# Kernel optimization log

Measured on AMD Instinct MI355X. Metric: run time of the kernel, lower is better.

Reference implementation:

```python
import jax, jax.numpy as jnp
import numpy as np

NUM_NODES = 50000
NUM_EDGES = 800000
NUM_LABEL_EDGES = 100000
F_IN, F_HID, F_OUT = 128, 128, 64


def gcn_conv(x, src, dst, W, b, n):
    # PyG GCNConv: h = x @ W; add self-loops; symmetric normalization
    # deg counted on destination (col), including self-loop (+1).
    h = x @ W
    deg = jax.ops.segment_sum(jnp.ones(src.shape, h.dtype), dst, num_segments=n) + 1.0
    dinv = jax.lax.rsqrt(deg)  # deg >= 1 always (self-loop)
    norm = dinv[src] * dinv[dst]                       # [E]
    agg = jax.ops.segment_sum(h[src] * norm[:, None], dst, num_segments=n)
    agg = agg + h * (dinv * dinv)[:, None]             # self-loop term dinv[i]^2 * h[i]
    return agg + b


def setup_inputs() -> dict:
    key = jax.random.key(0)
    ks = jax.random.split(key, 9)
    x = jax.random.normal(ks[0], (NUM_NODES, F_IN), dtype=jnp.float32)
    edge_index = jax.random.randint(ks[1], (2, NUM_EDGES), 0, NUM_NODES, dtype=jnp.int64)
    edge_label_index = jax.random.randint(ks[2], (2, NUM_LABEL_EDGES), 0, NUM_NODES, dtype=jnp.int64)
    def glorot(k, fi, fo):
        s = (6.0 / (fi + fo)) ** 0.5
        return jax.random.uniform(k, (fi, fo), jnp.float32, -s, s)
    return {
        "x": x,
        "edge_index": edge_index,
        "edge_label_index": edge_label_index,
        "W1": glorot(ks[3], F_IN, F_HID),  "b1": jnp.zeros((F_HID,), jnp.float32),
        "W2": glorot(ks[4], F_HID, F_HID), "b2": jnp.zeros((F_HID,), jnp.float32),
        "W3": glorot(ks[5], F_HID, F_OUT), "b3": jnp.zeros((F_OUT,), jnp.float32),
    }


def reference(x, edge_index, edge_label_index, W1, b1, W2, b2, W3, b3):
    src, dst = edge_index[0], edge_index[1]
    z = jax.nn.relu(gcn_conv(x, src, dst, W1, b1, NUM_NODES))
    z = jax.nn.relu(gcn_conv(z, src, dst, W2, b2, NUM_NODES))
    z = gcn_conv(z, src, dst, W3, b3, NUM_NODES)
    # decode: dot product of endpoint embeddings per label edge
    return jnp.sum(z[edge_label_index[0]] * z[edge_label_index[1]], axis=-1)
```

## Files before the change

### kernel.cpp

```cpp
#include <hip/hip_runtime.h>
#include <hip/hip_bf16.h>
#include <stdint.h>

#define NN 50000
#define NE 800000
#define NL 100000
#define SLOTS 64

#define NB 196
#define BSH 8
#define BCAP 5376

typedef __attribute__((ext_vector_type(8))) short bf16x8;
typedef __attribute__((ext_vector_type(4))) float f32x4;
typedef __attribute__((ext_vector_type(4))) unsigned int u32x4;

__device__ __forceinline__ float asf(unsigned int u) {
    union { unsigned int i; float f; } c; c.i = u; return c.f;
}
__device__ __forceinline__ float bflo(unsigned int x) { return asf(x << 16); }
__device__ __forceinline__ float bfhi(unsigned int x) { return asf(x & 0xffff0000u); }
__device__ __forceinline__ unsigned short f2bf(float f) {
    union { float f; unsigned int i; } c; c.f = f;
    unsigned int u = c.i + (0x7fffu + ((c.i >> 16) & 1u));
    return (unsigned short)(u >> 16);
}

__global__ void k_wprep(const float* __restrict__ W1, const float* __restrict__ W2,
                        const float* __restrict__ W3, unsigned short* __restrict__ Wt,
                        int* __restrict__ cursor) {
    int idx = blockIdx.x * 256 + threadIdx.x;
    if (idx < NB) cursor[idx] = 0;
    const float* W; unsigned short* O; int base, Mloc;
    if (idx < 16384)      { W = W1; O = Wt;         base = idx;         Mloc = 128; }
    else if (idx < 32768) { W = W2; O = Wt + 16384; base = idx - 16384; Mloc = 128; }
    else                  { W = W3; O = Wt + 32768; base = idx - 32768; Mloc = 64;  }
    int n = base >> 7, k = base & 127;
    O[base] = f2bf(W[k * Mloc + n]);
}

__global__ __launch_bounds__(256) void k_bin(
        const int* __restrict__ src, const int* __restrict__ dst,
        int* __restrict__ cursor, unsigned int* __restrict__ binbuf) {
    __shared__ int hcnt[NB];
    __shared__ int hbase[NB];
    __shared__ unsigned int epk[2048];
    int tid = threadIdx.x;
    if (tid < NB) hcnt[tid] = 0;
    __syncthreads();
    int e0 = blockIdx.x * 2048;
    int e1 = min(e0 + 2048, NE);
    for (int e = e0 + tid; e < e1; e += 256) {
        int d = dst[e], s = src[e];
        atomicAdd(&hcnt[d >> BSH], 1);
        epk[e - e0] = (unsigned int)s | ((unsigned int)d << 16);
    }
    __syncthreads();
    if (tid < NB) { hbase[tid] = atomicAdd(&cursor[tid], hcnt[tid]); hcnt[tid] = 0; }
    __syncthreads();
    for (int e = e0 + tid; e < e1; e += 256) {
        unsigned int pk = epk[e - e0];
        int b = (int)(pk >> 16) >> BSH;
        int p = hbase[b] + atomicAdd(&hcnt[b], 1);
        if (p < BCAP)
            __builtin_nontemporal_store(pk, &binbuf[(size_t)b * BCAP + p]);
    }
}

__global__ __launch_bounds__(256) void k_csr(
        const unsigned int* __restrict__ binbuf, const int* __restrict__ cursor,
        int* __restrict__ deg, unsigned short* __restrict__ colp) {
    __shared__ unsigned short lcol[256 * SLOTS];
    __shared__ int ldeg[256];
    int tid = threadIdx.x;
    int blk = blockIdx.x;
    int base = blk << BSH;
    int nNodes = min(256, NN - base);
    ldeg[tid] = 0;
    __syncthreads();
    int cnt = min(cursor[blk], BCAP);
    for (int e = tid; e < cnt; e += 256) {
        unsigned int pk = __builtin_nontemporal_load(&binbuf[(size_t)blk * BCAP + e]);
        int d = (int)(pk >> 16) - base;
        int p = atomicAdd(&ldeg[d], 1);
        if (p < SLOTS) lcol[d * SLOTS + p] = (unsigned short)(pk & 0xffffu);
    }
    __syncthreads();
    if (tid < nNodes) deg[base + tid] = ldeg[tid];
    u32x4* gout = (u32x4*)(colp + (size_t)base * SLOTS);
    const u32x4* lin = (const u32x4*)lcol;
    for (int i = tid; i < nNodes * 8; i += 256) gout[i] = lin[i];
}

__global__ __launch_bounds__(256) void k_gemm1(
        const float* __restrict__ A, const unsigned short* __restrict__ Wt,
        const int* __restrict__ deg, unsigned short* __restrict__ Outb, int N) {
    constexpr int K = 128;
    constexpr int NT = 8;
    int tid = threadIdx.x;
    int lane = tid & 63, wave = tid >> 6;
    int m = lane & 15, quad = lane >> 4;
    int rowA = blockIdx.x * 64 + wave * 16 + m;
    int rA = min(rowA, N - 1);

    bf16x8 afr[4];
    const float* p = A + (size_t)rA * K + quad * 8;
#pragma unroll
    for (int s = 0; s < 4; ++s) {
        float4 lo = *(const float4*)(p + s * 32);
        float4 hi = *(const float4*)(p + s * 32 + 4);
        bf16x8 r;
        r[0] = (short)f2bf(lo.x); r[1] = (short)f2bf(lo.y);
        r[2] = (short)f2bf(lo.z); r[3] = (short)f2bf(lo.w);
        r[4] = (short)f2bf(hi.x); r[5] = (short)f2bf(hi.y);
        r[6] = (short)f2bf(hi.z); r[7] = (short)f2bf(hi.w);
        afr[s] = r;
    }

    f32x4 acc[NT];
#pragma unroll
    for (int t = 0; t < NT; ++t) { acc[t][0] = 0.f; acc[t][1] = 0.f; acc[t][2] = 0.f; acc[t][3] = 0.f; }
#pragma unroll
    for (int t = 0; t < NT; ++t) {
        const unsigned short* wp = Wt + (size_t)(t * 16 + m) * K + quad * 8;
#pragma unroll
        for (int s = 0; s < 4; ++s) {
            bf16x8 bfr = *(const bf16x8*)(wp + s * 32);
            acc[t] = __builtin_amdgcn_mfma_f32_16x16x32_bf16(afr[s], bfr, acc[t], 0, 0, 0);
        }
    }

    int outRowBase = blockIdx.x * 64 + wave * 16 + quad * 4;
    float di[4];
#pragma unroll
    for (int i = 0; i < 4; ++i) di[i] = rsqrtf((float)deg[min(outRowBase + i, N - 1)] + 1.0f);
#pragma unroll
    for (int t = 0; t < NT; ++t)
#pragma unroll
        for (int i = 0; i < 4; ++i) {
            int rr = outRowBase + i;
            if (rr < N) Outb[(size_t)rr * 128 + t * 16 + m] = f2bf(acc[t][i] * di[i]);
        }
}

template <int M_>
__global__ __launch_bounds__(256) void k_agg_gemm(
        const unsigned short* __restrict__ hs, const int* __restrict__ deg,
        const unsigned short* __restrict__ colp, const float* __restrict__ bias,
        const unsigned short* __restrict__ Wt, unsigned short* __restrict__ Outb) {
    constexpr int K = 128;
    constexpr int NT = M_ / 64;
    __shared__ __align__(16) unsigned short As[16][136];
    int tid = threadIdx.x;
    int lane = tid & 63, wave = tid >> 6;
    int tileBase = blockIdx.x * 16;
    int g = lane >> 4, c = lane & 15;
    const unsigned short* hc = hs + c * 8;

    float bv[8];
    {
        const float4* bp = (const float4*)(bias + c * 8);
        float4 b0 = bp[0], b1 = bp[1];
        bv[0] = b0.x; bv[1] = b0.y; bv[2] = b0.z; bv[3] = b0.w;
        bv[4] = b1.x; bv[5] = b1.y; bv[6] = b1.z; bv[7] = b1.w;
    }

#pragma unroll
    for (int t = 0; t < 4; ++t) {
        int r = wave * 4 + t;
        int node = tileBase + r;
        int cnt = min(deg[node], SLOTS);
        int myIdx = (lane < cnt) ? (int)colp[(size_t)node * SLOTS + lane] : 0;

        float acc[8];
        {
            u32x4 v = {0, 0, 0, 0};
            if (g == 0) v = *(const u32x4*)(hc + (size_t)node * K);
#pragma unroll
            for (int k = 0; k < 4; ++k) { acc[2 * k] = bflo(v[k]); acc[2 * k + 1] = bfhi(v[k]); }
        }
        for (int j = 0; j < cnt; j += 8) {
            int i0 = __shfl(myIdx, j + g, 64);
            int i1 = __shfl(myIdx, j + 4 + g, 64);
            u32x4 v0 = {0, 0, 0, 0}, v1 = {0, 0, 0, 0};
            if (j + g < cnt)     v0 = *(const u32x4*)(hc + (size_t)i0 * K);
            if (j + 4 + g < cnt) v1 = *(const u32x4*)(hc + (size_t)i1 * K);
#pragma unroll
            for (int k = 0; k < 4; ++k) {
                acc[2 * k]     += bflo(v0[k]) + bflo(v1[k]);
                acc[2 * k + 1] += bfhi(v0[k]) + bfhi(v1[k]);
            }
        }
#pragma unroll
        for (int k = 0; k < 8; ++k) {
            acc[k] += __shfl_xor(acc[k], 16, 64);
            acc[k] += __shfl_xor(acc[k], 32, 64);
        }
        if (g == 0) {
            float di = rsqrtf((float)deg[node] + 1.0f);
            u32x4 pv;
#pragma unroll
            for (int k = 0; k < 4; ++k) {
                float o0 = fmaxf(di * acc[2 * k]     + bv[2 * k],     0.f);
                float o1 = fmaxf(di * acc[2 * k + 1] + bv[2 * k + 1], 0.f);
                pv[k] = (unsigned int)f2bf(o0) | ((unsigned int)f2bf(o1) << 16);
            }
            *(u32x4*)&As[r][c * 8] = pv;
        }
    }
    __syncthreads();

    int m = lane & 15, quad = lane >> 4;
    bf16x8 afr[4];
#pragma unroll
    for (int s = 0; s < 4; ++s)
        afr[s] = *(const bf16x8*)&As[m][s * 32 + quad * 8];

    f32x4 gacc[NT];
#pragma unroll
    for (int t = 0; t < NT; ++t) { gacc[t][0] = 0.f; gacc[t][1] = 0.f; gacc[t][2] = 0.f; gacc[t][3] = 0.f; }
#pragma unroll
    for (int t = 0; t < NT; ++t) {
        int ct = wave * NT + t;
        const unsigned short* wp = Wt + (size_t)(ct * 16 + m) * K + quad * 8;
#pragma unroll
        for (int s = 0; s < 4; ++s) {
            bf16x8 bfr = *(const bf16x8*)(wp + s * 32);
            gacc[t] = __builtin_amdgcn_mfma_f32_16x16x32_bf16(afr[s], bfr, gacc[t], 0, 0, 0);
        }
    }

    int rowBase = tileBase + quad * 4;
    float di[4];
#pragma unroll
    for (int i = 0; i < 4; ++i) di[i] = rsqrtf((float)deg[rowBase + i] + 1.0f);
#pragma unroll
    for (int t = 0; t < NT; ++t) {
        int ct = wave * NT + t;
#pragma unroll
        for (int i = 0; i < 4; ++i)
            Outb[(size_t)(rowBase + i) * M_ + ct * 16 + m] = f2bf(gacc[t][i] * di[i]);
    }
}

__global__ __launch_bounds__(256) void k_agg64(
        const unsigned short* __restrict__ hs, const int* __restrict__ deg,
        const unsigned short* __restrict__ colp, const float* __restrict__ bias,
        unsigned short* __restrict__ out, int n) {
    int tid = threadIdx.x;
    int wave = tid >> 6, lane = tid & 63;
    int node = blockIdx.x * 4 + wave;
    int g = lane >> 3, c = lane & 7;
    const unsigned short* hc = hs + c * 8;

    int cnt = min(deg[node], SLOTS);
    int myIdx = (lane < cnt) ? (int)colp[(size_t)node * SLOTS + lane] : 0;

    float acc[8];
    {
        u32x4 v = {0, 0, 0, 0};
        if (g == 0) v = *(const u32x4*)(hc + (size_t)node * 64);
#pragma unroll
        for (int k = 0; k < 4; ++k) { acc[2 * k] = bflo(v[k]); acc[2 * k + 1] = bfhi(v[k]); }
    }
    for (int j = 0; j < cnt; j += 16) {
        int i0 = __shfl(myIdx, j + g, 64);
        int i1 = __shfl(myIdx, j + 8 + g, 64);
        u32x4 v0 = {0, 0, 0, 0}, v1 = {0, 0, 0, 0};
        if (j + g < cnt)     v0 = *(const u32x4*)(hc + (size_t)i0 * 64);
        if (j + 8 + g < cnt) v1 = *(const u32x4*)(hc + (size_t)i1 * 64);
#pragma unroll
        for (int k = 0; k < 4; ++k) {
            acc[2 * k]     += bflo(v0[k]) + bflo(v1[k]);
            acc[2 * k + 1] += bfhi(v0[k]) + bfhi(v1[k]);
        }
    }
#pragma unroll
    for (int k = 0; k < 8; ++k) {
        acc[k] += __shfl_xor(acc[k], 8, 64);
        acc[k] += __shfl_xor(acc[k], 16, 64);
        acc[k] += __shfl_xor(acc[k], 32, 64);
    }
    if (g == 0) {
        float di = rsqrtf((float)deg[node] + 1.0f);
        const float4* bp = (const float4*)(bias + c * 8);
        float4 b0 = bp[0], b1 = bp[1];
        float bb[8] = {b0.x, b0.y, b0.z, b0.w, b1.x, b1.y, b1.z, b1.w};
        u32x4 pv;
#pragma unroll
        for (int k = 0; k < 4; ++k) {
            float o0 = di * acc[2 * k]     + bb[2 * k];
            float o1 = di * acc[2 * k + 1] + bb[2 * k + 1];
            pv[k] = (unsigned int)f2bf(o0) | ((unsigned int)f2bf(o1) << 16);
        }
        *(u32x4*)(out + (size_t)node * 64 + c * 8) = pv;
    }
}

__global__ __launch_bounds__(256) void k_decode(
        const unsigned short* __restrict__ z, const int* __restrict__ ls,
        const int* __restrict__ ld, float* __restrict__ out, int nl) {
    int tid = threadIdx.x;
    int lane = tid & 63, wave = tid >> 6;
    int g = lane >> 3, c = lane & 7;
    int e = (blockIdx.x * 4 + wave) * 4 + (g >> 1);
    int row = (g & 1) ? ld[e] : ls[e];
    u32x4 v = *(const u32x4*)(z + (size_t)row * 64 + c * 8);
    u32x4 w;
#pragma unroll
    for (int k = 0; k < 4; ++k) w[k] = (unsigned int)__shfl_xor((int)v[k], 8, 64);
    float p = 0.f;
#pragma unroll
    for (int k = 0; k < 4; ++k)
        p += bflo(v[k]) * bflo(w[k]) + bfhi(v[k]) * bfhi(w[k]);
    p += __shfl_xor(p, 1, 64);
    p += __shfl_xor(p, 2, 64);
    p += __shfl_xor(p, 4, 64);
    if ((lane & 15) == 0) out[e] = p;
}


static inline size_t align256(size_t x) { return (x + 255) & ~(size_t)255; }

extern "C" void kernel_launch(void* const* d_in, const int* in_sizes, int n_in,
                              void* d_out, int out_size, void* d_ws, size_t ws_size,
                              hipStream_t stream) {
    const float* x  = (const float*)d_in[0];
    const int*   ei = (const int*)d_in[1];
    const int*   li = (const int*)d_in[2];
    const float* W1 = (const float*)d_in[3];
    const float* b1 = (const float*)d_in[4];
    const float* W2 = (const float*)d_in[5];
    const float* b2 = (const float*)d_in[6];
    const float* W3 = (const float*)d_in[7];
    const float* b3 = (const float*)d_in[8];
    float* out = (float*)d_out;

    const int* src = ei;
    const int* dst = ei + NE;
    const int* ls = li;
    const int* ld = li + NL;

    char* ws = (char*)d_ws;
    size_t off = 0;
    int* deg    = (int*)(ws + off); off += align256(NN * 4);
    int* cursor = (int*)(ws + off); off += align256(NB * 4);
    unsigned int* binbuf = (unsigned int*)(ws + off); off += align256((size_t)NB * BCAP * 4);
    unsigned short* colp = (unsigned short*)(ws + off); off += align256((size_t)NN * SLOTS * 2);
    unsigned short* Wtb  = (unsigned short*)(ws + off); off += align256(40960 * 2);
    unsigned short* bufA = (unsigned short*)(ws + off); off += align256((size_t)NN * 128 * 2);
    unsigned short* bufB = (unsigned short*)(ws + off); off += align256((size_t)NN * 128 * 2);
    unsigned short* bufZ = (unsigned short*)(ws + off); off += align256((size_t)NN * 64 * 2);

    k_wprep<<<160, 256, 0, stream>>>(W1, W2, W3, Wtb, cursor);
    k_bin<<<391, 256, 0, stream>>>(src, dst, cursor, binbuf);
    k_csr<<<NB, 256, 0, stream>>>(binbuf, cursor, deg, colp);

    k_gemm1<<<782, 256, 0, stream>>>(x, Wtb, deg, bufA, NN);
    k_agg_gemm<128><<<3125, 256, 0, stream>>>(bufA, deg, colp, b1, Wtb + 16384, bufB);
    k_agg_gemm<64><<<3125, 256, 0, stream>>>(bufB, deg, colp, b2, Wtb + 32768, bufA);
    k_agg64<<<12500, 256, 0, stream>>>(bufA, deg, colp, b3, bufZ, NN);
    k_decode<<<6250, 256, 0, stream>>>(bufZ, ls, ld, out, NL);
}
```

Before: 249.5 us.

## Issue all neighbor gathers up front with masked unconditional loads in aggregation

Aggregation kernels now load eight column indices per lane group as a vector and issue all neighbor row gathers unconditionally before accumulating. Invalid slots are masked to zero rather than branched around, which relies on k_csr now zero-filling the column table so padded indices point at node 0. The aim is to raise memory-level parallelism and remove the serial shuffle/load loop, at the cost of wasted loads for low-degree nodes and more registers. In k_agg64 the degree is clamped to 64 and all slots are covered, so high-degree nodes no longer need a tail loop there. k_agg_gemm keeps a tail loop for degrees above 32, and both kernels now compute the normalization from the clamped degree.

```diff
diff --git a/kernel.cpp b/kernel.cpp
--- a/kernel.cpp
+++ b/kernel.cpp
@@ -14,6 +14,7 @@
 typedef __attribute__((ext_vector_type(8))) short bf16x8;
 typedef __attribute__((ext_vector_type(4))) float f32x4;
 typedef __attribute__((ext_vector_type(4))) unsigned int u32x4;
+typedef __attribute__((ext_vector_type(8))) unsigned short u16x8;
 
 __device__ __forceinline__ float asf(unsigned int u) {
     union { unsigned int i; float f; } c; c.i = u; return c.f;
@@ -77,6 +78,9 @@
     int base = blk << BSH;
     int nNodes = min(256, NN - base);
     ldeg[tid] = 0;
+    u32x4* lz = (u32x4*)lcol;
+#pragma unroll
+    for (int i = 0; i < 8; ++i) lz[i * 256 + tid] = (u32x4){0, 0, 0, 0};
     __syncthreads();
     int cnt = min(cursor[blk], BCAP);
     for (int e = tid; e < cnt; e += 256) {
@@ -156,6 +160,7 @@
     int tileBase = blockIdx.x * 16;
     int g = lane >> 4, c = lane & 15;
     const unsigned short* hc = hs + c * 8;
+    int nodeB = tileBase + wave * 4;
 
     float bv[8];
     {
@@ -165,39 +170,66 @@
         bv[4] = b1.x; bv[5] = b1.y; bv[6] = b1.z; bv[7] = b1.w;
     }
 
+    int cnt[4];
+    u16x8 sl[4];
+#pragma unroll
+    for (int t = 0; t < 4; ++t) cnt[t] = min(deg[nodeB + t], SLOTS);
+#pragma unroll
+    for (int t = 0; t < 4; ++t)
+        sl[t] = *(const u16x8*)(colp + (size_t)(nodeB + t) * SLOTS + g * 8);
+
+    unsigned int smk = (g == 0) ? 0xffffffffu : 0u;
+
 #pragma unroll
     for (int t = 0; t < 4; ++t) {
         int r = wave * 4 + t;
-        int node = tileBase + r;
-        int cnt = min(deg[node], SLOTS);
-        int myIdx = (lane < cnt) ? (int)colp[(size_t)node * SLOTS + lane] : 0;
+        int node = nodeB + t;
+
+        u32x4 sv = *(const u32x4*)(hc + (size_t)node * K);
+        u32x4 vv[8];
+        unsigned int mk[8];
+#pragma unroll
+        for (int k2 = 0; k2 < 8; ++k2) {
+            int slot = g * 8 + k2;
+            mk[k2] = (slot < cnt[t]) ? 0xffffffffu : 0u;
+            vv[k2] = *(const u32x4*)(hc + (size_t)(int)sl[t][k2] * K);
+        }
 
         float acc[8];
-        {
-            u32x4 v = {0, 0, 0, 0};
-            if (g == 0) v = *(const u32x4*)(hc + (size_t)node * K);
-#pragma unroll
-            for (int k = 0; k < 4; ++k) { acc[2 * k] = bflo(v[k]); acc[2 * k + 1] = bfhi(v[k]); }
-        }
-        for (int j = 0; j < cnt; j += 8) {
-            int i0 = __shfl(myIdx, j + g, 64);
-            int i1 = __shfl(myIdx, j + 4 + g, 64);
-            u32x4 v0 = {0, 0, 0, 0}, v1 = {0, 0, 0, 0};
-            if (j + g < cnt)     v0 = *(const u32x4*)(hc + (size_t)i0 * K);
-            if (j + 4 + g < cnt) v1 = *(const u32x4*)(hc + (size_t)i1 * K);
+#pragma unroll
+        for (int k = 0; k < 4; ++k) {
+            unsigned int xv = sv[k] & smk;
+            acc[2 * k] = bflo(xv); acc[2 * k + 1] = bfhi(xv);
+        }
+#pragma unroll
+        for (int k2 = 0; k2 < 8; ++k2) {
 #pragma unroll
             for (int k = 0; k < 4; ++k) {
-                acc[2 * k]     += bflo(v0[k]) + bflo(v1[k]);
-                acc[2 * k + 1] += bfhi(v0[k]) + bfhi(v1[k]);
+                unsigned int xv = vv[k2][k] & mk[k2];
+                acc[2 * k] += bflo(xv); acc[2 * k + 1] += bfhi(xv);
             }
         }
+
+        if (cnt[t] > 32) {
+            int mi = (lane < cnt[t]) ? (int)colp[(size_t)node * SLOTS + lane] : 0;
+            for (int j = 32; j < cnt[t]; j += 4) {
+                int i0 = __shfl(mi, j + g, 64);
+                u32x4 v0 = {0, 0, 0, 0};
+                if (j + g < cnt[t]) v0 = *(const u32x4*)(hc + (size_t)i0 * K);
+#pragma unroll
+                for (int k = 0; k < 4; ++k) {
+                    acc[2 * k] += bflo(v0[k]); acc[2 * k + 1] += bfhi(v0[k]);
+                }
+            }
+        }
+
 #pragma unroll
         for (int k = 0; k < 8; ++k) {
             acc[k] += __shfl_xor(acc[k], 16, 64);
             acc[k] += __shfl_xor(acc[k], 32, 64);
         }
         if (g == 0) {
-            float di = rsqrtf((float)deg[node] + 1.0f);
+            float di = rsqrtf((float)cnt[t] + 1.0f);
             u32x4 pv;
 #pragma unroll
             for (int k = 0; k < 4; ++k) {
@@ -254,25 +286,31 @@
     const unsigned short* hc = hs + c * 8;
 
     int cnt = min(deg[node], SLOTS);
-    int myIdx = (lane < cnt) ? (int)colp[(size_t)node * SLOTS + lane] : 0;
-
+    u16x8 sl = *(const u16x8*)(colp + (size_t)node * SLOTS + g * 8);
+
+    u32x4 sv = *(const u32x4*)(hc + (size_t)node * 64);
+    u32x4 vv[8];
+    unsigned int mk[8];
+#pragma unroll
+    for (int k2 = 0; k2 < 8; ++k2) {
+        int slot = g * 8 + k2;
+        mk[k2] = (slot < cnt) ? 0xffffffffu : 0u;
+        vv[k2] = *(const u32x4*)(hc + (size_t)(int)sl[k2] * 64);
+    }
+
+    unsigned int smk = (g == 0) ? 0xffffffffu : 0u;
     float acc[8];
-    {
-        u32x4 v = {0, 0, 0, 0};
-        if (g == 0) v = *(const u32x4*)(hc + (size_t)node * 64);
-#pragma unroll
-        for (int k = 0; k < 4; ++k) { acc[2 * k] = bflo(v[k]); acc[2 * k + 1] = bfhi(v[k]); }
-    }
-    for (int j = 0; j < cnt; j += 16) {
-        int i0 = __shfl(myIdx, j + g, 64);
-        int i1 = __shfl(myIdx, j + 8 + g, 64);
-        u32x4 v0 = {0, 0, 0, 0}, v1 = {0, 0, 0, 0};
-        if (j + g < cnt)     v0 = *(const u32x4*)(hc + (size_t)i0 * 64);
-        if (j + 8 + g < cnt) v1 = *(const u32x4*)(hc + (size_t)i1 * 64);
+#pragma unroll
+    for (int k = 0; k < 4; ++k) {
+        unsigned int xv = sv[k] & smk;
+        acc[2 * k] = bflo(xv); acc[2 * k + 1] = bfhi(xv);
+    }
+#pragma unroll
+    for (int k2 = 0; k2 < 8; ++k2) {
 #pragma unroll
         for (int k = 0; k < 4; ++k) {
-            acc[2 * k]     += bflo(v0[k]) + bflo(v1[k]);
-            acc[2 * k + 1] += bfhi(v0[k]) + bfhi(v1[k]);
+            unsigned int xv = vv[k2][k] & mk[k2];
+            acc[2 * k] += bflo(xv); acc[2 * k + 1] += bfhi(xv);
         }
     }
 #pragma unroll
@@ -282,7 +320,7 @@
         acc[k] += __shfl_xor(acc[k], 32, 64);
     }
     if (g == 0) {
-        float di = rsqrtf((float)deg[node] + 1.0f);
+        float di = rsqrtf((float)cnt + 1.0f);
         const float4* bp = (const float4*)(bias + c * 8);
         float4 b0 = bp[0], b1 = bp[1];
         float bb[8] = {b0.x, b0.y, b0.z, b0.w, b1.x, b1.y, b1.z, b1.w};
```

Result: faster. 240.6 us (-3.6%).

## Split features into 32-wide slices and use padded fixed-slot branchless aggregation

Applied to the files above, without the earlier changes.

Transformed features are now stored as four 32-column slices in separate planes, so each aggregation block gathers one 64-byte row slice per neighbor and the gather working set fits better in cache. Neighbor lists are padded with a pointer to a zeroed pad row, and the self-loop is inserted as a slot. This lets aggregation issue 32 unconditional gathers up front, with a second 32 only for high-degree nodes. The fused aggregate+GEMM kernels are split back into separate aggregation and GEMM launches, which adds an intermediate buffer round-trip and extra launches.

```diff
diff --git a/kernel.cpp b/kernel.cpp
--- a/kernel.cpp
+++ b/kernel.cpp
@@ -6,10 +6,13 @@
 #define NE 800000
 #define NL 100000
 #define SLOTS 64
+#define PADROW 50000
 
 #define NB 196
 #define BSH 8
 #define BCAP 5376
+
+#define SL (50001u * 32u)
 
 typedef __attribute__((ext_vector_type(8))) short bf16x8;
 typedef __attribute__((ext_vector_type(4))) float f32x4;
@@ -28,9 +31,14 @@
 
 __global__ void k_wprep(const float* __restrict__ W1, const float* __restrict__ W2,
                         const float* __restrict__ W3, unsigned short* __restrict__ Wt,
-                        int* __restrict__ cursor) {
+                        int* __restrict__ cursor, unsigned short* __restrict__ bufH) {
     int idx = blockIdx.x * 256 + threadIdx.x;
     if (idx < NB) cursor[idx] = 0;
+    if (idx < 64) {
+        int sl = idx >> 4, w = idx & 15;
+        unsigned int* pw = (unsigned int*)(bufH + (size_t)sl * SL + (size_t)PADROW * 32);
+        pw[w] = 0;
+    }
     const float* W; unsigned short* O; int base, Mloc;
     if (idx < 16384)      { W = W1; O = Wt;         base = idx;         Mloc = 128; }
     else if (idx < 32768) { W = W2; O = Wt + 16384; base = idx - 16384; Mloc = 128; }
@@ -77,6 +85,11 @@
     int base = blk << BSH;
     int nNodes = min(256, NN - base);
     ldeg[tid] = 0;
+    const unsigned int fw = 0xC350C350u;
+    u32x4 fill = {fw, fw, fw, fw};
+    u32x4* lz = (u32x4*)lcol;
+#pragma unroll
+    for (int i = 0; i < 8; ++i) lz[i * 256 + tid] = fill;
     __syncthreads();
     int cnt = min(cursor[blk], BCAP);
     for (int e = tid; e < cnt; e += 256) {
@@ -86,7 +99,13 @@
         if (p < SLOTS) lcol[d * SLOTS + p] = (unsigned short)(pk & 0xffffu);
     }
     __syncthreads();
-    if (tid < nNodes) deg[base + tid] = ldeg[tid];
+    if (tid < nNodes) {
+        int dv = ldeg[tid];
+        deg[base + tid] = dv;
+        if (dv < SLOTS)
+            lcol[tid * SLOTS + dv] = (unsigned short)(base + tid);
+    }
+    __syncthreads();
     u32x4* gout = (u32x4*)(colp + (size_t)base * SLOTS);
     const u32x4* lin = (const u32x4*)lcol;
     for (int i = tid; i < nNodes * 8; i += 256) gout[i] = lin[i];
@@ -139,161 +158,138 @@
 #pragma unroll
         for (int i = 0; i < 4; ++i) {
             int rr = outRowBase + i;
-            if (rr < N) Outb[(size_t)rr * 128 + t * 16 + m] = f2bf(acc[t][i] * di[i]);
+            if (rr < N)
+                Outb[(size_t)(t >> 1) * SL + (size_t)rr * 32 + (t & 1) * 16 + m] =
+                    f2bf(acc[t][i] * di[i]);
         }
 }
 
 template <int M_>
-__global__ __launch_bounds__(256) void k_agg_gemm(
-        const unsigned short* __restrict__ hs, const int* __restrict__ deg,
+__global__ __launch_bounds__(256) void k_gemmb(
+        const unsigned short* __restrict__ A, const unsigned short* __restrict__ Wt,
+        const int* __restrict__ deg, unsigned short* __restrict__ Outb, int N) {
+    constexpr int K = 128;
+    constexpr int NT = M_ / 16;
+    int tid = threadIdx.x;
+    int lane = tid & 63, wave = tid >> 6;
+    int m = lane & 15, quad = lane >> 4;
+    int rowA = blockIdx.x * 64 + wave * 16 + m;
+    int rA = min(rowA, N - 1);
+
+    bf16x8 afr[4];
+#pragma unroll
+    for (int s = 0; s < 4; ++s)
+        afr[s] = *(const bf16x8*)(A + (size_t)rA * K + quad * 8 + s * 32);
+
+    f32x4 acc[NT];
+#pragma unroll
+    for (int t = 0; t < NT; ++t) { acc[t][0] = 0.f; acc[t][1] = 0.f; acc[t][2] = 0.f; acc[t][3] = 0.f; }
+#pragma unroll
+    for (int t = 0; t < NT; ++t) {
+        const unsigned short* wp = Wt + (size_t)(t * 16 + m) * K + quad * 8;
+#pragma unroll
+        for (int s = 0; s < 4; ++s) {
+            bf16x8 bfr = *(const bf16x8*)(wp + s * 32);
+            acc[t] = __builtin_amdgcn_mfma_f32_16x16x32_bf16(afr[s], bfr, acc[t], 0, 0, 0);
+        }
+    }
+
+    int outRowBase = blockIdx.x * 64 + wave * 16 + quad * 4;
+    float di[4];
+#pragma unroll
+    for (int i = 0; i < 4; ++i) di[i] = rsqrtf((float)deg[min(outRowBase + i, N - 1)] + 1.0f);
+#pragma unroll
+    for (int t = 0; t < NT; ++t)
+#pragma unroll
+        for (int i = 0; i < 4; ++i) {
+            int rr = outRowBase + i;
+            if (rr < N)
+                Outb[(size_t)(t >> 1) * SL + (size_t)rr * 32 + (t & 1) * 16 + m] =
+                    f2bf(acc[t][i] * di[i]);
+        }
+}
+
+template <int NS, bool RELU>
+__global__ __launch_bounds__(256) void k_aggs(
+        const unsigned short* __restrict__ hsl, const int* __restrict__ deg,
         const unsigned short* __restrict__ colp, const float* __restrict__ bias,
-        const unsigned short* __restrict__ Wt, unsigned short* __restrict__ Outb) {
-    constexpr int K = 128;
-    constexpr int NT = M_ / 64;
-    __shared__ __align__(16) unsigned short As[16][136];
-    int tid = threadIdx.x;
-    int lane = tid & 63, wave = tid >> 6;
-    int tileBase = blockIdx.x * 16;
-    int g = lane >> 4, c = lane & 15;
-    const unsigned short* hc = hs + c * 8;
-
-    float bv[8];
+        unsigned short* __restrict__ z) {
+    constexpr int ZW = NS * 32;
+    int tid = threadIdx.x;
+    int wave = tid >> 6, lane = tid & 63;
+    int r4 = lane >> 2, c4 = lane & 3;
+    int p = blockIdx.x / 3125;
+    int tb = (blockIdx.x % 3125) * 16;
+    int nodeB = tb + wave * 4;
+    const unsigned short* hp = hsl + (size_t)p * SL;
+
+    int4 dg = *(const int4*)(deg + nodeB);
+    int dgv[4] = {dg.x, dg.y, dg.z, dg.w};
+
+    float bb[8];
     {
-        const float4* bp = (const float4*)(bias + c * 8);
+        const float4* bp = (const float4*)(bias + p * 32 + c4 * 8);
         float4 b0 = bp[0], b1 = bp[1];
-        bv[0] = b0.x; bv[1] = b0.y; bv[2] = b0.z; bv[3] = b0.w;
-        bv[4] = b1.x; bv[5] = b1.y; bv[6] = b1.z; bv[7] = b1.w;
-    }
+        bb[0] = b0.x; bb[1] = b0.y; bb[2] = b0.z; bb[3] = b0.w;
+        bb[4] = b1.x; bb[5] = b1.y; bb[6] = b1.z; bb[7] = b1.w;
+    }
+
+    unsigned int idx[8];
+#pragma unroll
+    for (int t = 0; t < 4; ++t)
+#pragma unroll
+        for (int b = 0; b < 2; ++b)
+            idx[t * 2 + b] = colp[(unsigned)(nodeB + t) * SLOTS + b * 16 + r4];
+
+    u32x4 v[8];
+#pragma unroll
+    for (int j = 0; j < 8; ++j)
+        v[j] = *(const u32x4*)(hp + (size_t)idx[j] * 32 + c4 * 8);
 
 #pragma unroll
     for (int t = 0; t < 4; ++t) {
-        int r = wave * 4 + t;
-        int node = tileBase + r;
-        int cnt = min(deg[node], SLOTS);
-        int myIdx = (lane < cnt) ? (int)colp[(size_t)node * SLOTS + lane] : 0;
-
+        int node = nodeB + t;
         float acc[8];
-        {
-            u32x4 v = {0, 0, 0, 0};
-            if (g == 0) v = *(const u32x4*)(hc + (size_t)node * K);
-#pragma unroll
-            for (int k = 0; k < 4; ++k) { acc[2 * k] = bflo(v[k]); acc[2 * k + 1] = bfhi(v[k]); }
-        }
-        for (int j = 0; j < cnt; j += 8) {
-            int i0 = __shfl(myIdx, j + g, 64);
-            int i1 = __shfl(myIdx, j + 4 + g, 64);
-            u32x4 v0 = {0, 0, 0, 0}, v1 = {0, 0, 0, 0};
-            if (j + g < cnt)     v0 = *(const u32x4*)(hc + (size_t)i0 * K);
-            if (j + 4 + g < cnt) v1 = *(const u32x4*)(hc + (size_t)i1 * K);
+#pragma unroll
+        for (int k = 0; k < 8; ++k) acc[k] = 0.f;
+#pragma unroll
+        for (int b = 0; b < 2; ++b)
 #pragma unroll
             for (int k = 0; k < 4; ++k) {
-                acc[2 * k]     += bflo(v0[k]) + bflo(v1[k]);
-                acc[2 * k + 1] += bfhi(v0[k]) + bfhi(v1[k]);
+                acc[2 * k]     += bflo(v[t * 2 + b][k]);
+                acc[2 * k + 1] += bfhi(v[t * 2 + b][k]);
             }
+        if (dgv[t] > 31) {
+#pragma unroll
+            for (int b = 2; b < 4; ++b) {
+                unsigned int ix = colp[(unsigned)node * SLOTS + b * 16 + r4];
+                u32x4 w = *(const u32x4*)(hp + (size_t)ix * 32 + c4 * 8);
+#pragma unroll
+                for (int k = 0; k < 4; ++k) {
+                    acc[2 * k]     += bflo(w[k]);
+                    acc[2 * k + 1] += bfhi(w[k]);
+                }
+            }
         }
 #pragma unroll
         for (int k = 0; k < 8; ++k) {
+            acc[k] += __shfl_xor(acc[k], 4, 64);
+            acc[k] += __shfl_xor(acc[k], 8, 64);
             acc[k] += __shfl_xor(acc[k], 16, 64);
             acc[k] += __shfl_xor(acc[k], 32, 64);
         }
-        if (g == 0) {
-            float di = rsqrtf((float)deg[node] + 1.0f);
+        if (r4 == 0) {
+            float di = rsqrtf((float)dgv[t] + 1.0f);
             u32x4 pv;
 #pragma unroll
             for (int k = 0; k < 4; ++k) {
-                float o0 = fmaxf(di * acc[2 * k]     + bv[2 * k],     0.f);
-                float o1 = fmaxf(di * acc[2 * k + 1] + bv[2 * k + 1], 0.f);
+                float o0 = di * acc[2 * k]     + bb[2 * k];
+                float o1 = di * acc[2 * k + 1] + bb[2 * k + 1];
+                if (RELU) { o0 = fmaxf(o0, 0.f); o1 = fmaxf(o1, 0.f); }
                 pv[k] = (unsigned int)f2bf(o0) | ((unsigned int)f2bf(o1) << 16);
             }
-            *(u32x4*)&As[r][c * 8] = pv;
-        }
-    }
-    __syncthreads();
-
-    int m = lane & 15, quad = lane >> 4;
-    bf16x8 afr[4];
-#pragma unroll
-    for (int s = 0; s < 4; ++s)
-        afr[s] = *(const bf16x8*)&As[m][s * 32 + quad * 8];
-
-    f32x4 gacc[NT];
-#pragma unroll
-    for (int t = 0; t < NT; ++t) { gacc[t][0] = 0.f; gacc[t][1] = 0.f; gacc[t][2] = 0.f; gacc[t][3] = 0.f; }
-#pragma unroll
-    for (int t = 0; t < NT; ++t) {
-        int ct = wave * NT + t;
-        const unsigned short* wp = Wt + (size_t)(ct * 16 + m) * K + quad * 8;
-#pragma unroll
-        for (int s = 0; s < 4; ++s) {
-            bf16x8 bfr = *(const bf16x8*)(wp + s * 32);
-            gacc[t] = __builtin_amdgcn_mfma_f32_16x16x32_bf16(afr[s], bfr, gacc[t], 0, 0, 0);
-        }
-    }
-
-    int rowBase = tileBase + quad * 4;
-    float di[4];
-#pragma unroll
-    for (int i = 0; i < 4; ++i) di[i] = rsqrtf((float)deg[rowBase + i] + 1.0f);
-#pragma unroll
-    for (int t = 0; t < NT; ++t) {
-        int ct = wave * NT + t;
-#pragma unroll
-        for (int i = 0; i < 4; ++i)
-            Outb[(size_t)(rowBase + i) * M_ + ct * 16 + m] = f2bf(gacc[t][i] * di[i]);
-    }
-}
-
-__global__ __launch_bounds__(256) void k_agg64(
-        const unsigned short* __restrict__ hs, const int* __restrict__ deg,
-        const unsigned short* __restrict__ colp, const float* __restrict__ bias,
-        unsigned short* __restrict__ out, int n) {
-    int tid = threadIdx.x;
-    int wave = tid >> 6, lane = tid & 63;
-    int node = blockIdx.x * 4 + wave;
-    int g = lane >> 3, c = lane & 7;
-    const unsigned short* hc = hs + c * 8;
-
-    int cnt = min(deg[node], SLOTS);
-    int myIdx = (lane < cnt) ? (int)colp[(size_t)node * SLOTS + lane] : 0;
-
-    float acc[8];
-    {
-        u32x4 v = {0, 0, 0, 0};
-        if (g == 0) v = *(const u32x4*)(hc + (size_t)node * 64);
-#pragma unroll
-        for (int k = 0; k < 4; ++k) { acc[2 * k] = bflo(v[k]); acc[2 * k + 1] = bfhi(v[k]); }
-    }
-    for (int j = 0; j < cnt; j += 16) {
-        int i0 = __shfl(myIdx, j + g, 64);
-        int i1 = __shfl(myIdx, j + 8 + g, 64);
-        u32x4 v0 = {0, 0, 0, 0}, v1 = {0, 0, 0, 0};
-        if (j + g < cnt)     v0 = *(const u32x4*)(hc + (size_t)i0 * 64);
-        if (j + 8 + g < cnt) v1 = *(const u32x4*)(hc + (size_t)i1 * 64);
-#pragma unroll
-        for (int k = 0; k < 4; ++k) {
-            acc[2 * k]     += bflo(v0[k]) + bflo(v1[k]);
-            acc[2 * k + 1] += bfhi(v0[k]) + bfhi(v1[k]);
-        }
-    }
-#pragma unroll
-    for (int k = 0; k < 8; ++k) {
-        acc[k] += __shfl_xor(acc[k], 8, 64);
-        acc[k] += __shfl_xor(acc[k], 16, 64);
-        acc[k] += __shfl_xor(acc[k], 32, 64);
-    }
-    if (g == 0) {
-        float di = rsqrtf((float)deg[node] + 1.0f);
-        const float4* bp = (const float4*)(bias + c * 8);
-        float4 b0 = bp[0], b1 = bp[1];
-        float bb[8] = {b0.x, b0.y, b0.z, b0.w, b1.x, b1.y, b1.z, b1.w};
-        u32x4 pv;
-#pragma unroll
-        for (int k = 0; k < 4; ++k) {
-            float o0 = di * acc[2 * k]     + bb[2 * k];
-            float o1 = di * acc[2 * k + 1] + bb[2 * k + 1];
-            pv[k] = (unsigned int)f2bf(o0) | ((unsigned int)f2bf(o1) << 16);
-        }
-        *(u32x4*)(out + (size_t)node * 64 + c * 8) = pv;
+            *(u32x4*)(z + (size_t)node * ZW + p * 32 + c4 * 8) = pv;
+        }
     }
 }
 
@@ -348,17 +344,19 @@
     unsigned int* binbuf = (unsigned int*)(ws + off); off += align256((size_t)NB * BCAP * 4);
     unsigned short* colp = (unsigned short*)(ws + off); off += align256((size_t)NN * SLOTS * 2);
     unsigned short* Wtb  = (unsigned short*)(ws + off); off += align256(40960 * 2);
-    unsigned short* bufA = (unsigned short*)(ws + off); off += align256((size_t)NN * 128 * 2);
-    unsigned short* bufB = (unsigned short*)(ws + off); off += align256((size_t)NN * 128 * 2);
-    unsigned short* bufZ = (unsigned short*)(ws + off); off += align256((size_t)NN * 64 * 2);
-
-    k_wprep<<<160, 256, 0, stream>>>(W1, W2, W3, Wtb, cursor);
+    unsigned short* bufH = (unsigned short*)(ws + off); off += align256((size_t)4 * SL * 2);
+    unsigned short* bufZ1 = (unsigned short*)(ws + off); off += align256((size_t)NN * 128 * 2);
+    unsigned short* bufZZ = (unsigned short*)(ws + off); off += align256((size_t)NN * 64 * 2);
+
+    k_wprep<<<160, 256, 0, stream>>>(W1, W2, W3, Wtb, cursor, bufH);
     k_bin<<<391, 256, 0, stream>>>(src, dst, cursor, binbuf);
     k_csr<<<NB, 256, 0, stream>>>(binbuf, cursor, deg, colp);
 
-    k_gemm1<<<782, 256, 0, stream>>>(x, Wtb, deg, bufA, NN);
-    k_agg_gemm<128><<<3125, 256, 0, stream>>>(bufA, deg, colp, b1, Wtb + 16384, bufB);
-    k_agg_gemm<64><<<3125, 256, 0, stream>>>(bufB, deg, colp, b2, Wtb + 32768, bufA);
-    k_agg64<<<12500, 256, 0, stream>>>(bufA, deg, colp, b3, bufZ, NN);
-    k_decode<<<6250, 256, 0, stream>>>(bufZ, ls, ld, out, NL);
-}
+    k_gemm1<<<782, 256, 0, stream>>>(x, Wtb, deg, bufH, NN);
+    k_aggs<4, true><<<12500, 256, 0, stream>>>(bufH, deg, colp, b1, bufZ1);
+    k_gemmb<128><<<782, 256, 0, stream>>>(bufZ1, Wtb + 16384, deg, bufH, NN);
+    k_aggs<4, true><<<12500, 256, 0, stream>>>(bufH, deg, colp, b2, bufZ1);
+    k_gemmb<64><<<782, 256, 0, stream>>>(bufZ1, Wtb + 32768, deg, bufH, NN);
+    k_aggs<2, false><<<6250, 256, 0, stream>>>(bufH, deg, colp, b3, bufZZ);
+    k_decode<<<6250, 256, 0, stream>>>(bufZZ, ls, ld, out, NL);
+}
```

Result: slower. 354.0 us (+41.9%).
